# Performance work log

Hardware: AMD Instinct MI355X
Metric: run time of the kernel (lower is better)

## Reference

```python
import jax, jax.numpy as jnp
import numpy as np

N_HEADS, N_LEVELS, N_POINTS, D_MODEL = 8, 3, 12, 64
PARAM_NAMES = ['vp0_w','vp0_b','vp1_w','vp1_b','so0_w','so0_b','so1_w','so1_b','so2_w','so2_b','so3_w','so3_b','aw0_w','aw0_b','aw1_w','aw1_b','aw2_w','aw2_b','aw3_w','aw3_b','op0_w','op0_b','op1_w','op1_b']

def _lrelu(x):
    return jnp.where(x >= 0, x, 0.1 * x)

def _conv(x, w, b):
    y = jax.lax.conv_general_dilated(x, w, (1, 1), 'SAME', dimension_numbers=('NCHW', 'OIHW', 'NCHW'))
    return y + b[None, :, None, None]

def _bilinear(img, px, py):
    # img [B,C,H,W]; px,py [B,Q] absolute pixel coords; zero padding (grid_sample 'zeros')
    B, C, H, W = img.shape
    flat = img.reshape(B, C, H * W)
    x0 = jnp.floor(px); y0 = jnp.floor(py)
    wx1 = px - x0; wy1 = py - y0
    def g(xi, yi, wgt):
        valid = (xi >= 0) & (xi <= W - 1) & (yi >= 0) & (yi <= H - 1)
        xi_c = jnp.clip(xi, 0, W - 1).astype(jnp.int32)
        yi_c = jnp.clip(yi, 0, H - 1).astype(jnp.int32)
        v = jnp.take_along_axis(flat, (yi_c * W + xi_c)[:, None, :], axis=2)
        return v * (wgt * valid)[:, None, :]
    return (g(x0, y0, (1 - wx1) * (1 - wy1)) + g(x0 + 1, y0, wx1 * (1 - wy1))
          + g(x0, y0 + 1, (1 - wx1) * wy1) + g(x0 + 1, y0 + 1, wx1 * wy1))

def _flow_warp(img, flow):
    # img [n,C,h,w]; flow [n,2,h,w] (x,y); matches grid_sample align_corners=True
    n, C, h, w = img.shape
    gy, gx = jnp.meshgrid(jnp.arange(h, dtype=img.dtype), jnp.arange(w, dtype=img.dtype), indexing='ij')
    px = (gx[None] + flow[:, 0]).reshape(n, h * w)
    py = (gy[None] + flow[:, 1]).reshape(n, h * w)
    return _bilinear(img, px, py).reshape(n, C, h, w)

def _forward(x, flow_1, flow_2, flip_flow_1, flip_flow_2, p):
    n, t, c, h, w = x.shape
    hw = h * w; THW = t * hw
    M, L, P, D = N_HEADS, N_LEVELS, N_POINTS, c // N_HEADS
    flow_cn1 = flow_1
    flow_cn2 = flow_1 + _flow_warp(flow_2, flow_1)
    flow_n1c, flow_n1n2 = flip_flow_1, flow_2
    flow_n2n1 = flip_flow_2
    flow_n2c = flip_flow_2 + _flow_warp(flip_flow_1, flip_flow_2)
    warp_cn1 = _flow_warp(x[:, 1], flow_cn1)
    warp_cn2 = _flow_warp(x[:, 2], flow_cn2)
    warp_n1c = _flow_warp(x[:, 0], flow_n1c)
    warp_n1n2 = _flow_warp(x[:, 2], flow_n1n2)
    warp_n2n1 = _flow_warp(x[:, 1], flow_n2n1)
    warp_n2c = _flow_warp(x[:, 0], flow_n2c)
    extra = jnp.concatenate([x[:, 0], warp_cn1, warp_cn2, warp_n1c, warp_n1n2, warp_n2n1, warp_n2c,
                             flow_cn1, flow_cn2, flow_n1c, flow_n1n2, flow_n2n1, flow_n2c], axis=1)
    value = _conv(_lrelu(_conv(x.reshape(n, t * c, h, w), p['vp0_w'], p['vp0_b'])), p['vp1_w'], p['vp1_b'])
    def head(e, pre):
        y = _lrelu(_conv(e, p[pre + '0_w'], p[pre + '0_b']))
        y = _lrelu(_conv(y, p[pre + '1_w'], p[pre + '1_b']))
        y = _lrelu(_conv(y, p[pre + '2_w'], p[pre + '2_b']))
        return _conv(y, p[pre + '3_w'], p[pre + '3_b'])
    so = head(extra, 'so')  # [n, L*M*L*P*2, h, w]
    aw = head(extra, 'aw')  # [n, L*M*L*P*9, h, w]
    so = so.reshape(n, t, -1, hw).transpose(0, 1, 3, 2).reshape(n, THW, M, L, P, 2)
    aw = aw.reshape(n, t, -1, hw).transpose(0, 1, 3, 2).reshape(n, THW, M, L * P * 9)
    aw = jax.nn.softmax(aw, axis=-1).reshape(n, THW, M, L, P * 9)
    # flow-guided offsets: add per-(query-frame, target-level) flow to learned offsets
    off = so.reshape(n, t, hw, M, L, P, 2)
    fz = jnp.zeros_like(flow_cn2)
    def lvl(f0, f1, f2):
        s = jnp.stack([f0, f1, f2], 1)  # [n,3,2,h,w]
        return s.transpose(0, 3, 4, 1, 2).reshape(n, hw, L, 2)[:, None, :, None, :, None, :]
    off = jnp.concatenate([
        off[:, 0:1] + lvl(fz, flow_cn1, flow_cn2),
        off[:, 1:2] + lvl(flow_n1c, fz, flow_n1n2),
        off[:, 2:3] + lvl(flow_n2c, flow_n2n1, fz)], axis=1).reshape(n, THW, M, L, P, 2)
    # 3x3 integer patch around each sampling point
    pi, pj = jnp.meshgrid(jnp.arange(-1, 2), jnp.arange(-1, 2), indexing='ij')
    patch = jnp.stack([pi, pj], -1).reshape(1, 1, 1, 1, 1, 9, 2).astype(off.dtype)
    off = (off[..., None, :] + patch).reshape(n, THW, M, L, P * 9, 2)
    # reference points (valid_ratios are all 1: full masks are zeros)
    ry, rx = jnp.meshgrid((jnp.arange(h) + 0.5) / h, (jnp.arange(w) + 0.5) / w, indexing='ij')
    ref = jnp.stack([rx, ry], -1).reshape(1, hw, 2).astype(off.dtype)
    ref = jnp.tile(ref, (1, t, 1))  # [1, THW, 2]
    norm = jnp.array([w, h], dtype=off.dtype)
    loc = ref[:, :, None, None, None, :] + off / norm  # [n,THW,M,L,P*9,2] normalized
    # multi-scale deformable attention (all L levels share (h,w)); align_corners=False, zeros pad
    P9 = P * 9
    v = value.reshape(n, t, c, hw).transpose(0, 1, 3, 2).reshape(n, THW, M, D)
    vl = v.reshape(n, L, hw, M, D).transpose(0, 3, 1, 4, 2).reshape(n * M * L, D, h, w)
    px = (loc[..., 0] * w - 0.5).transpose(0, 2, 3, 1, 4).reshape(n * M * L, THW * P9)
    py = (loc[..., 1] * h - 0.5).transpose(0, 2, 3, 1, 4).reshape(n * M * L, THW * P9)
    sampled = _bilinear(vl, px, py).reshape(n, M, L, D, THW, P9)
    out = jnp.einsum('nmldqp,nqmlp->nqmd', sampled, aw).reshape(n, THW, c)
    out = out.reshape(n, t, h, w, c).transpose(0, 1, 4, 2, 3).reshape(n, t * c, h, w)
    out = _conv(_lrelu(_conv(out, p['op0_w'], p['op0_b'])), p['op1_w'], p['op1_b'])
    return out.reshape(n, t, c, h, w) + x

def setup_inputs():
    key = jax.random.key(0)
    n, t, c, h, w = 1, 3, 64, 32, 32
    ks = jax.random.split(key, 24)
    d = {}
    d['x'] = jax.random.normal(ks[0], (n, t, c, h, w), jnp.float32)
    for i, name in enumerate(['flow_1', 'flow_2', 'flip_flow_1', 'flip_flow_2']):
        d[name] = jax.random.normal(ks[1 + i], (n, 2, h, w), jnp.float32)
    cin_extra = 7 * c + 12
    specs = [('vp0', t * c, t * c), ('vp1', t * c, t * c),
             ('so0', c, cin_extra), ('so1', c, c), ('so2', c, c), ('so3', N_LEVELS * N_HEADS * N_LEVELS * N_POINTS * 2, c),
             ('aw0', c, cin_extra), ('aw1', c, c), ('aw2', c, c), ('aw3', N_LEVELS * N_HEADS * N_LEVELS * N_POINTS * 9, c),
             ('op0', t * c, t * c), ('op1', t * c, t * c)]
    for i, (name, co, ci) in enumerate(specs):
        kw, kb = jax.random.split(ks[5 + i])
        std = (2.0 / (ci * 9)) ** 0.5
        d[name + '_w'] = jax.random.normal(kw, (co, ci, 3, 3), jnp.float32) * std
        d[name + '_b'] = jax.random.normal(kb, (co,), jnp.float32) * 0.01
    return d

def reference(x, flow_1, flow_2, flip_flow_1, flip_flow_2, vp0_w, vp0_b, vp1_w, vp1_b, so0_w, so0_b, so1_w, so1_b, so2_w, so2_b, so3_w, so3_b, aw0_w, aw0_b, aw1_w, aw1_b, aw2_w, aw2_b, aw3_w, aw3_b, op0_w, op0_b, op1_w, op1_b):
    p = dict(zip(PARAM_NAMES, (vp0_w, vp0_b, vp1_w, vp1_b, so0_w, so0_b, so1_w, so1_b, so2_w, so2_b, so3_w, so3_b, aw0_w, aw0_b, aw1_w, aw1_b, aw2_w, aw2_b, aw3_w, aw3_b, op0_w, op0_b, op1_w, op1_b)))
    return _forward(x, flow_1, flow_2, flip_flow_1, flip_flow_2, p)
```

## Files before the change

### kernel.cpp

```cpp
#include <hip/hip_runtime.h>
#include <math.h>

#define HW 1024

typedef __attribute__((ext_vector_type(8))) short bf16x8;
typedef __attribute__((ext_vector_type(4))) float floatx4;

__device__ __forceinline__ unsigned short f2bf(float f) {
    unsigned u = __float_as_uint(f);
    u += 0x7FFF + ((u >> 16) & 1);
    return (unsigned short)(u >> 16);
}
__device__ __forceinline__ float bf2f(unsigned short u) {
    return __uint_as_float(((unsigned)u) << 16);
}
__device__ __forceinline__ float bflo(unsigned u) { return __uint_as_float(u << 16); }
__device__ __forceinline__ float bfhi(unsigned u) { return __uint_as_float(u & 0xffff0000u); }

__device__ __forceinline__ float bilin32(const float* __restrict__ img, float px, float py) {
    float x0f = floorf(px), y0f = floorf(py);
    float wx = px - x0f, wy = py - y0f;
    bool vx0 = (x0f >= 0.f) && (x0f <= 31.f);
    bool vx1 = (x0f >= -1.f) && (x0f <= 30.f);
    bool vy0 = (y0f >= 0.f) && (y0f <= 31.f);
    bool vy1 = (y0f >= -1.f) && (y0f <= 30.f);
    int ix0 = (int)fminf(fmaxf(x0f, 0.f), 31.f);
    int iy0 = (int)fminf(fmaxf(y0f, 0.f), 31.f);
    int ix1 = (int)fminf(fmaxf(x0f + 1.f, 0.f), 31.f);
    int iy1 = (int)fminf(fmaxf(y0f + 1.f, 0.f), 31.f);
    float w00 = (1.f - wx) * (1.f - wy) * ((vx0 && vy0) ? 1.f : 0.f);
    float w01 = wx * (1.f - wy) * ((vx1 && vy0) ? 1.f : 0.f);
    float w10 = (1.f - wx) * wy * ((vx0 && vy1) ? 1.f : 0.f);
    float w11 = wx * wy * ((vx1 && vy1) ? 1.f : 0.f);
    return w00 * img[iy0 * 32 + ix0] + w01 * img[iy0 * 32 + ix1] +
           w10 * img[iy1 * 32 + ix0] + w11 * img[iy1 * 32 + ix1];
}

__device__ __forceinline__ float2 comp_flow(const float* __restrict__ fa,
                                            const float* __restrict__ fb, int pix) {
    int y = pix >> 5, x = pix & 31;
    float fx = fa[pix], fy = fa[HW + pix];
    float px = (float)x + fx, py = (float)y + fy;
    float2 r;
    r.x = fx + bilin32(fb, px, py);
    r.y = fy + bilin32(fb + HW, px, py);
    return r;
}

struct WD { const float* src; int cout, Cin, nCb, wbase, beg; };
struct PrepP {
    const float *x, *f1, *f2, *ff1, *ff2;
    float *fcn2, *fn2c;
    unsigned short *x_pad, *extra_pad, *wgt;
    WD wd[12];
};

__global__ __launch_bounds__(256) void prep_k(PrepP P) {
    __shared__ float wlds[16 * 288];
    const int b = blockIdx.x, tid = threadIdx.x;
    if (b < 192) {
        int idx = b * 256 + tid;
        int pix = idx / 48, c4 = idx - pix * 48;
        int y = pix >> 5, xx = pix & 31;
        int c0 = c4 * 4;
        ushort4 s;
        s.x = f2bf(P.x[(size_t)(c0 + 0) * HW + pix]);
        s.y = f2bf(P.x[(size_t)(c0 + 1) * HW + pix]);
        s.z = f2bf(P.x[(size_t)(c0 + 2) * HW + pix]);
        s.w = f2bf(P.x[(size_t)(c0 + 3) * HW + pix]);
        *(ushort4*)(&P.x_pad[(size_t)((y + 1) * 34 + xx + 1) * 192 + c0]) = s;
    } else if (b < 2112) {
        int idx = (b - 192) * 256 + tid;
        int ch = idx >> 10, pix = idx & 1023;
        int y = pix >> 5, xx = pix & 31;
        float v = 0.f;
        if (ch < 64) {
            v = P.x[(size_t)ch * HW + pix];
        } else if (ch < 448) {
            int grp = (ch - 64) >> 6;
            int c = (ch - 64) & 63;
            const float* src;
            float fx, fy;
            if (grp == 0)      { src = P.x + 64 * HW;  fx = P.f1[pix];  fy = P.f1[HW + pix]; }
            else if (grp == 1) { src = P.x + 128 * HW; float2 r = comp_flow(P.f1, P.f2, pix);  fx = r.x; fy = r.y; }
            else if (grp == 2) { src = P.x;            fx = P.ff1[pix]; fy = P.ff1[HW + pix]; }
            else if (grp == 3) { src = P.x + 128 * HW; fx = P.f2[pix];  fy = P.f2[HW + pix]; }
            else if (grp == 4) { src = P.x + 64 * HW;  fx = P.ff2[pix]; fy = P.ff2[HW + pix]; }
            else               { src = P.x;            float2 r = comp_flow(P.ff2, P.ff1, pix); fx = r.x; fy = r.y; }
            v = bilin32(src + c * HW, (float)xx + fx, (float)y + fy);
        } else if (ch < 460) {
            int fc = ch - 448;
            int which = fc >> 1, comp = fc & 1;
            if (which == 0)      v = P.f1[comp * HW + pix];
            else if (which == 1) { float2 r = comp_flow(P.f1, P.f2, pix);  v = comp ? r.y : r.x; }
            else if (which == 2) v = P.ff1[comp * HW + pix];
            else if (which == 3) v = P.f2[comp * HW + pix];
            else if (which == 4) v = P.ff2[comp * HW + pix];
            else                 { float2 r = comp_flow(P.ff2, P.ff1, pix); v = comp ? r.y : r.x; }
        }
        P.extra_pad[(size_t)((y + 1) * 34 + xx + 1) * 480 + ch] = f2bf(v);
    } else if (b < 2128) {
        int idx = (b - 2112) * 256 + tid;
        if (idx < 1024) {
            float2 r = comp_flow(P.f1, P.f2, idx);
            P.fcn2[idx] = r.x; P.fcn2[HW + idx] = r.y;
        } else if (idx < 2048) {
            int pix = idx - 1024;
            float2 r = comp_flow(P.ff2, P.ff1, pix);
            P.fn2c[pix] = r.x; P.fn2c[HW + pix] = r.y;
        }
    } else if (b < 2144) {
        const int chans[9] = {192, 192, 480, 64, 64, 64, 64, 192, 192};
        size_t offs[9]; size_t a = 0;
        for (int i = 0; i < 9; ++i) { offs[i] = a; a += (size_t)1156 * chans[i]; }
        int bb = b - 2128;
        for (int item = bb; item < 9 * 132; item += 16) {
            int buf = item / 132, i = item - buf * 132;
            int py, px;
            if (i < 34) { py = 0; px = i; }
            else if (i < 68) { py = 33; px = i - 34; }
            else { int j = i - 68; py = 1 + (j >> 1); px = (j & 1) ? 33 : 0; }
            int C = chans[buf];
            unsigned short* p = P.x_pad + offs[buf] + (size_t)(py * 34 + px) * C;
            for (int c = tid; c < C; c += 256) p[c] = 0;
        }
    } else {
        int blk = b - 2144;
        int di = 0;
        while (di < 11 && blk >= P.wd[di + 1].beg) ++di;
        WD w = P.wd[di];
        int local = blk - w.beg;
        int co16 = local / w.nCb, cb = local - co16 * w.nCb;
        int cr0 = co16 * 16, ci0 = cb * 32;
        for (int i = tid; i < 16 * 288; i += 256) {
            int cr = i / 288, o = i - cr * 288;
            int crg = cr0 + cr, ci = ci0 + o / 9;
            float v = (crg < w.cout && ci < w.Cin)
                ? w.src[((size_t)crg * w.Cin + ci0) * 9 + o] : 0.f;
            wlds[i] = v;
        }
        __syncthreads();
        for (int e = tid; e < 9 * 512; e += 256) {
            int t = e >> 9, idx = e & 511;
            int j = idx & 7, lane = idx >> 3, q = lane >> 4, mm = lane & 15;
            P.wgt[((size_t)w.wbase + ((size_t)co16 * 9 + t) * w.nCb + cb) * 512 + idx] =
                f2bf(wlds[mm * 288 + (q * 8 + j) * 9 + t]);
        }
    }
}

struct CDesc {
    const unsigned short* in;
    const unsigned short* wgt;
    const float* bias;
    void* out;
    const float* residual;
    int Cpad, nCb, Cout, mode, cmod, relu, Mblocks;
};
struct CParam { CDesc d[4]; };

template<int PIXROWS, int COBLK>
__global__ __launch_bounds__(256) void conv_mfma_k(CParam P) {
    constexpr int TROWS = PIXROWS + 2;
    constexpr int TC = TROWS * 34 * 4;
    constexpr int ITRIPS = (TC + 255) / 256;
    constexpr int NTY = PIXROWS / 4;
    constexpr int NACC = NTY * 2;
    constexpr int MT = COBLK / 16;
    constexpr int WN = MT * 9 * 64;
    constexpr int WTRIPS = (WN + 255) / 256;
    __shared__ unsigned short blds[TROWS * 34 * 40];
    __shared__ unsigned short wlds[MT * 9 * 512];

    int bx = blockIdx.x;
    int di = 0;
    while (bx >= P.d[di].Mblocks) { bx -= P.d[di].Mblocks; ++di; }
    const CDesc d = P.d[di];

    const int tid = threadIdx.x;
    const int w = tid >> 6, lane = tid & 63;
    const int lq = lane >> 4, ln = lane & 15;
    const int co0 = bx * COBLK;
    const int by = blockIdx.y, y0 = by * PIXROWS;
    const unsigned short* __restrict__ in = d.in;
    const unsigned short* __restrict__ wg = d.wgt;
    const int Cpad = d.Cpad, nCb = d.nCb;

    floatx4 acc[MT][NACC];
#pragma unroll
    for (int mt = 0; mt < MT; ++mt)
#pragma unroll
        for (int nt = 0; nt < NACC; ++nt)
            acc[mt][nt] = (floatx4){0.f, 0.f, 0.f, 0.f};

    bf16x8 ireg[ITRIPS];
    bf16x8 wreg[WTRIPS];

    auto load_regs = [&](int cb) {
        const int ci0 = cb << 5;
#pragma unroll
        for (int k = 0; k < ITRIPS; ++k) {
            int i = tid + k * 256;
            if (i < TC) {
                int r = i / 136, rem = i - r * 136, c = rem >> 2, g = rem & 3;
                ireg[k] = *(const bf16x8*)(in + (size_t)((y0 + r) * 34 + c) * Cpad + ci0 + g * 8);
            }
        }
#pragma unroll
        for (int k = 0; k < WTRIPS; ++k) {
            int i = tid + k * 256;
            if (i < WN) {
                int chunk = i >> 6, l16 = i & 63;
                int mt = chunk / 9, t = chunk - mt * 9;
                wreg[k] = *(const bf16x8*)(wg + ((size_t)(((co0 >> 4) + mt) * 9 + t) * nCb + cb) * 512 + l16 * 8);
            }
        }
// ... 55 lines not shown
            const int pix = by * (PIXROWS * 32) + (w * NTY + ty) * 32 + tx * 16 + ln;
            float v[4];
#pragma unroll
            for (int r = 0; r < 4; ++r) {
                float vv = acc[mt][nt][r] + bv[r];
                if (d.relu) vv = (vv >= 0.f) ? vv : 0.1f * vv;
                v[r] = vv;
            }
            if (d.mode == 0) {
                float* o = (float*)d.out;
#pragma unroll
                for (int r = 0; r < 4; ++r) {
                    float vv = v[r];
                    if (d.residual) vv += d.residual[(size_t)(co + r) * HW + pix];
                    o[(size_t)(co + r) * HW + pix] = vv;
                }
            } else if (d.mode == 1) {
                int fq = co / d.cmod, cc = co - fq * d.cmod;
                *(float4*)((float*)d.out + ((size_t)fq * HW + pix) * d.cmod + cc) =
                    make_float4(v[0], v[1], v[2], v[3]);
            } else if (d.mode == 2) {
                int fq = co / d.cmod, cc = co - fq * d.cmod;
                ushort4 s4;
                s4.x = f2bf(v[0]); s4.y = f2bf(v[1]); s4.z = f2bf(v[2]); s4.w = f2bf(v[3]);
                *(ushort4*)((unsigned short*)d.out + ((size_t)fq * HW + pix) * d.cmod + cc) = s4;
            } else {
                int yy = (pix >> 5) + 1, xx = (pix & 31) + 1;
                ushort4 s4;
                s4.x = f2bf(v[0]); s4.y = f2bf(v[1]); s4.z = f2bf(v[2]); s4.w = f2bf(v[3]);
                *(ushort4*)((unsigned short*)d.out + (size_t)(yy * 34 + xx) * d.cmod + co) = s4;
            }
        }
    }
}

__global__ __launch_bounds__(256) void deform_attn_k(
    const unsigned short* __restrict__ value_b, const float* __restrict__ so_t,
    const unsigned short* __restrict__ aw_t,
    const float* __restrict__ flow_1, const float* __restrict__ flow_2,
    const float* __restrict__ flip_flow_1, const float* __restrict__ flip_flow_2,
    const float* __restrict__ flow_cn2, const float* __restrict__ flow_n2c,
    unsigned short* __restrict__ attn_pad)
{
    __shared__ unsigned short vlds[24576];
    __shared__ unsigned short pwlds[4][432];
    const int tid = threadIdx.x;
    const int wav = tid >> 6, lane = tid & 63;
    const int m = blockIdx.x & 7, qc = blockIdx.x >> 3;

    for (int i = tid; i < 3072; i += 256) {
        int l = i >> 10, p = i & 1023;
        *(bf16x8*)(&vlds[(size_t)i * 8]) =
            *(const bf16x8*)(value_b + ((size_t)((l * 8 + m) * 1024) + p) * 8);
    }
    __syncthreads();

    const int pp = lane & 15, gq = lane >> 4;
    const int gdy = (gq >> 1) * 2 - 1;
    const int gdx = (gq & 1) * 2 - 1;
    const bool selx = (gq & 1);
    const bool sely = (gq >> 1);

    for (int r = 0; r < 8; ++r) {
        const int q = qc * 32 + r * 4 + wav;
        const int f = q >> 10, pix = q & 1023;
        const int y = pix >> 5, x = pix & 31;

        float flx0 = 0.f, fly0 = 0.f, flx1 = 0.f, fly1 = 0.f, flx2 = 0.f, fly2 = 0.f;
        if (f == 0) {
            flx1 = flow_1[pix];      fly1 = flow_1[HW + pix];
            flx2 = flow_cn2[pix];    fly2 = flow_cn2[HW + pix];
        } else if (f == 1) {
            flx0 = flip_flow_1[pix]; fly0 = flip_flow_1[HW + pix];
            flx2 = flow_2[pix];      fly2 = flow_2[HW + pix];
        } else {
            flx0 = flow_n2c[pix];    fly0 = flow_n2c[HW + pix];
            flx1 = flip_flow_2[pix]; fly1 = flip_flow_2[HW + pix];
        }

        const unsigned short* awp = aw_t + (size_t)q * 2592 + m * 324;
        float av[6];
        float vmax = -1e30f;
// ... 86 lines not shown
                        int px = min(max(x0 + dx, 0), 31);
                        int py = min(max(y0 + dy, 0), 31);
                        float c = cg[sy][sx] * (v ? 1.f : 0.f);
                        uint4 vv = *(const uint4*)(&vlds[(size_t)(vbase + py * 32 + px) * 8]);
                        acc[0] = fmaf(c, bflo(vv.x), acc[0]);
                        acc[1] = fmaf(c, bfhi(vv.x), acc[1]);
                        acc[2] = fmaf(c, bflo(vv.y), acc[2]);
                        acc[3] = fmaf(c, bfhi(vv.y), acc[3]);
                        acc[4] = fmaf(c, bflo(vv.z), acc[4]);
                        acc[5] = fmaf(c, bfhi(vv.z), acc[5]);
                        acc[6] = fmaf(c, bflo(vv.w), acc[6]);
                        acc[7] = fmaf(c, bfhi(vv.w), acc[7]);
                    }
                }
            }
        }

#pragma unroll
        for (int dd = 0; dd < 8; ++dd) {
#pragma unroll
            for (int off = 32; off; off >>= 1) acc[dd] += __shfl_xor(acc[dd], off);
        }
        if (lane == 0) {
            unsigned short* op = attn_pad + (size_t)((y + 1) * 34 + x + 1) * 192 + f * 64 + m * 8;
            ushort4 s0, s1;
            s0.x = f2bf(acc[0]); s0.y = f2bf(acc[1]); s0.z = f2bf(acc[2]); s0.w = f2bf(acc[3]);
            s1.x = f2bf(acc[4]); s1.y = f2bf(acc[5]); s1.z = f2bf(acc[6]); s1.w = f2bf(acc[7]);
            *(ushort4*)(op) = s0;
            *(ushort4*)(op + 4) = s1;
        }
    }
}

extern "C" void kernel_launch(void* const* d_in, const int* in_sizes, int n_in,
                              void* d_out, int out_size, void* d_ws, size_t ws_size,
                              hipStream_t stream) {
    const float* x      = (const float*)d_in[0];
    const float* flow_1 = (const float*)d_in[1];
    const float* flow_2 = (const float*)d_in[2];
    const float* flip_1 = (const float*)d_in[3];
    const float* flip_2 = (const float*)d_in[4];
    const float* vp0_w = (const float*)d_in[5];  const float* vp0_b = (const float*)d_in[6];
    const float* vp1_w = (const float*)d_in[7];  const float* vp1_b = (const float*)d_in[8];
    const float* so0_w = (const float*)d_in[9];  const float* so0_b = (const float*)d_in[10];
    const float* so1_w = (const float*)d_in[11]; const float* so1_b = (const float*)d_in[12];
    const float* so2_w = (const float*)d_in[13]; const float* so2_b = (const float*)d_in[14];
    const float* so3_w = (const float*)d_in[15]; const float* so3_b = (const float*)d_in[16];
    const float* aw0_w = (const float*)d_in[17]; const float* aw0_b = (const float*)d_in[18];
    const float* aw1_w = (const float*)d_in[19]; const float* aw1_b = (const float*)d_in[20];
    const float* aw2_w = (const float*)d_in[21]; const float* aw2_b = (const float*)d_in[22];
    const float* aw3_w = (const float*)d_in[23]; const float* aw3_b = (const float*)d_in[24];
    const float* op0_w = (const float*)d_in[25]; const float* op0_b = (const float*)d_in[26];
    const float* op1_w = (const float*)d_in[27]; const float* op1_b = (const float*)d_in[28];
    float* out = (float*)d_out;
    (void)ws_size; (void)in_sizes; (void)n_in; (void)out_size;

    float* fws = (float*)d_ws;
    float* flow_cn2 = fws;
    float* flow_n2c = flow_cn2 + 2048;
    unsigned short* value_b = (unsigned short*)(flow_n2c + 2048);
    float* so_t     = (float*)(value_b + 196608);
    unsigned short* uws = (unsigned short*)(so_t + 1769472);
    unsigned short* x_pad     = uws;
    unsigned short* vp0h      = x_pad + 1156 * 192;
    unsigned short* extra_pad = vp0h + 1156 * 192;
    unsigned short* s1 = extra_pad + 1156 * 480;
    unsigned short* a1 = s1 + 1156 * 64;
    unsigned short* s2 = a1 + 1156 * 64;
    unsigned short* a2 = s2 + 1156 * 64;
    unsigned short* attn_pad = a2 + 1156 * 64;
    unsigned short* op0h     = attn_pad + 1156 * 192;
    unsigned short* aw_t = op0h + 1156 * 192;
    unsigned short* wgt  = aw_t + (size_t)3072 * 2592;

    PrepP pp;
    pp.x = x; pp.f1 = flow_1; pp.f2 = flow_2; pp.ff1 = flip_1; pp.ff2 = flip_2;
    pp.fcn2 = flow_cn2; pp.fn2c = flow_n2c;
    pp.x_pad = x_pad; pp.extra_pad = extra_pad; pp.wgt = wgt;
    pp.wd[0]  = {vp0_w, 192, 192, 6,     0,    0};
    pp.wd[1]  = {vp1_w, 192, 192, 6,   648,   72};
    pp.wd[2]  = {so0_w,  64, 460, 15, 1296,  144};
    pp.wd[3]  = {aw0_w,  64, 460, 15, 1836,  204};
    pp.wd[4]  = {so1_w,  64,  64, 2,  2376,  264};
    pp.wd[5]  = {aw1_w,  64,  64, 2,  2448,  272};
    pp.wd[6]  = {so2_w,  64,  64, 2,  2520,  280};
    pp.wd[7]  = {aw2_w,  64,  64, 2,  2592,  288};
    pp.wd[8]  = {so3_w, 1728, 64, 2,  2664,  296};
    pp.wd[9]  = {aw3_w, 7776, 64, 2,  4608,  512};
    pp.wd[10] = {op0_w, 192, 192, 6, 13392, 1488};
    pp.wd[11] = {op1_w, 192, 192, 6, 14040, 1560};
    prep_k<<<3776, 256, 0, stream>>>(pp);

    const int BIG = 1 << 30;
    CDesc nul = {nullptr, nullptr, nullptr, nullptr, nullptr, 0, 0, 0, 0, 0, 0, BIG};

    {
        CParam cp;
        cp.d[0] = {x_pad,     wgt + (size_t)0 * 512,    vp0_b, vp0h, nullptr, 192, 6,  192, 3, 192, 1, 12};
        cp.d[1] = {extra_pad, wgt + (size_t)1296 * 512, so0_b, s1,   nullptr, 480, 15, 64,  3, 64,  1, 4};
        cp.d[2] = {extra_pad, wgt + (size_t)1836 * 512, aw0_b, a1,   nullptr, 480, 15, 64,  3, 64,  1, 4};
        cp.d[3] = nul;
        conv_mfma_k<4, 16><<<dim3(20, 8), 256, 0, stream>>>(cp);
    }
    {
        CParam cp;
        cp.d[0] = {vp0h, wgt + (size_t)648 * 512,  vp1_b, value_b, nullptr, 192, 6, 192, 2, 8,  0, 12};
        cp.d[1] = {s1,   wgt + (size_t)2376 * 512, so1_b, s2,      nullptr, 64,  2, 64,  3, 64, 1, 4};
        cp.d[2] = {a1,   wgt + (size_t)2448 * 512, aw1_b, a2,      nullptr, 64,  2, 64,  3, 64, 1, 4};
        cp.d[3] = nul;
        conv_mfma_k<4, 16><<<dim3(20, 8), 256, 0, stream>>>(cp);
    }
    {
        CParam cp;
        cp.d[0] = {s2, wgt + (size_t)2520 * 512, so2_b, s1, nullptr, 64, 2, 64, 3, 64, 1, 4};
        cp.d[1] = {a2, wgt + (size_t)2592 * 512, aw2_b, a1, nullptr, 64, 2, 64, 3, 64, 1, 4};
        cp.d[2] = nul; cp.d[3] = nul;
        conv_mfma_k<4, 16><<<dim3(8, 8), 256, 0, stream>>>(cp);
    }
    {
        CParam cp;
        cp.d[0] = {s1, wgt + (size_t)2664 * 512, so3_b, so_t, nullptr, 64, 2, 1728, 1, 576,  0, 27};
        cp.d[1] = {a1, wgt + (size_t)4608 * 512, aw3_b, aw_t, nullptr, 64, 2, 7776, 2, 2592, 0, 122};
        cp.d[2] = nul; cp.d[3] = nul;
        conv_mfma_k<8, 64><<<dim3(149, 4), 256, 0, stream>>>(cp);
    }

    deform_attn_k<<<768, 256, 0, stream>>>(value_b, so_t, aw_t,
                                           flow_1, flow_2, flip_1, flip_2,
                                           flow_cn2, flow_n2c, attn_pad);

    {
        CParam cp;
        cp.d[0] = {attn_pad, wgt + (size_t)13392 * 512, op0_b, op0h, nullptr, 192, 6, 192, 3, 192, 1, 12};
        cp.d[1] = nul; cp.d[2] = nul; cp.d[3] = nul;
        conv_mfma_k<4, 16><<<dim3(12, 8), 256, 0, stream>>>(cp);
    }
    {
        CParam cp;
        cp.d[0] = {op0h, wgt + (size_t)14040 * 512, op1_b, out, x, 192, 6, 192, 0, 0, 0, 12};
        cp.d[1] = nul; cp.d[2] = nul; cp.d[3] = nul;
        conv_mfma_k<4, 16><<<dim3(12, 8), 256, 0, stream>>>(cp);
    }
}
```

Before: 269.9 us.

## Fuse all stages into persistent megakernel with software grid barriers

```diff
diff --git a/kernel.cpp b/kernel.cpp
--- a/kernel.cpp
+++ b/kernel.cpp
@@ -2,6 +2,8 @@
 #include <math.h>
 
 #define HW 1024
+#define GRID 768
+#define SMEM_BYTES 52608
 
 typedef __attribute__((ext_vector_type(8))) short bf16x8;
 typedef __attribute__((ext_vector_type(4))) float floatx4;
@@ -47,67 +49,82 @@
     return r;
 }
 
-struct WD { const float* src; int cout, Cin, nCb, wbase, beg; };
-struct PrepP {
-    const float *x, *f1, *f2, *ff1, *ff2;
-    float *fcn2, *fn2c;
-    unsigned short *x_pad, *extra_pad, *wgt;
-    WD wd[12];
+struct MegaA {
+    const float* x;
+    const float* f1; const float* f2; const float* ff1; const float* ff2;
+    const float* wp[24];
+    float* out;
+    char* ws;
+    int* bar;
 };
 
-__global__ __launch_bounds__(256) void prep_k(PrepP P) {
-    __shared__ float wlds[16 * 288];
-    const int b = blockIdx.x, tid = threadIdx.x;
+__device__ __forceinline__ void grid_bar(int* bar, int phase) {
+    __syncthreads();
+    if (threadIdx.x == 0) {
+        __threadfence();
+        __hip_atomic_fetch_add(bar + phase * 16, 1, __ATOMIC_ACQ_REL, __HIP_MEMORY_SCOPE_AGENT);
+        while (__hip_atomic_load(bar + phase * 16, __ATOMIC_RELAXED, __HIP_MEMORY_SCOPE_AGENT) < GRID)
+            __builtin_amdgcn_s_sleep(8);
+        __threadfence();
+    }
+    __syncthreads();
+}
+
+__device__ __forceinline__ void prep_tile(const MegaA& A, float* fcn2, float* fn2c,
+                                          unsigned short* x_pad, unsigned short* extra_pad,
+                                          unsigned short* wgt, int b, char* smraw) {
+    const int tid = threadIdx.x;
+    const float* x = A.x;
     if (b < 192) {
         int idx = b * 256 + tid;
         int pix = idx / 48, c4 = idx - pix * 48;
         int y = pix >> 5, xx = pix & 31;
         int c0 = c4 * 4;
         ushort4 s;
-        s.x = f2bf(P.x[(size_t)(c0 + 0) * HW + pix]);
-        s.y = f2bf(P.x[(size_t)(c0 + 1) * HW + pix]);
-        s.z = f2bf(P.x[(size_t)(c0 + 2) * HW + pix]);
-        s.w = f2bf(P.x[(size_t)(c0 + 3) * HW + pix]);
-        *(ushort4*)(&P.x_pad[(size_t)((y + 1) * 34 + xx + 1) * 192 + c0]) = s;
+        s.x = f2bf(x[(size_t)(c0 + 0) * HW + pix]);
+        s.y = f2bf(x[(size_t)(c0 + 1) * HW + pix]);
+        s.z = f2bf(x[(size_t)(c0 + 2) * HW + pix]);
+        s.w = f2bf(x[(size_t)(c0 + 3) * HW + pix]);
+        *(ushort4*)(&x_pad[(size_t)((y + 1) * 34 + xx + 1) * 192 + c0]) = s;
     } else if (b < 2112) {
         int idx = (b - 192) * 256 + tid;
         int ch = idx >> 10, pix = idx & 1023;
         int y = pix >> 5, xx = pix & 31;
         float v = 0.f;
         if (ch < 64) {
-            v = P.x[(size_t)ch * HW + pix];
+            v = x[(size_t)ch * HW + pix];
         } else if (ch < 448) {
             int grp = (ch - 64) >> 6;
             int c = (ch - 64) & 63;
             const float* src;
             float fx, fy;
-            if (grp == 0)      { src = P.x + 64 * HW;  fx = P.f1[pix];  fy = P.f1[HW + pix]; }
-            else if (grp == 1) { src = P.x + 128 * HW; float2 r = comp_flow(P.f1, P.f2, pix);  fx = r.x; fy = r.y; }
-            else if (grp == 2) { src = P.x;            fx = P.ff1[pix]; fy = P.ff1[HW + pix]; }
-            else if (grp == 3) { src = P.x + 128 * HW; fx = P.f2[pix];  fy = P.f2[HW + pix]; }
-            else if (grp == 4) { src = P.x + 64 * HW;  fx = P.ff2[pix]; fy = P.ff2[HW + pix]; }
-            else               { src = P.x;            float2 r = comp_flow(P.ff2, P.ff1, pix); fx = r.x; fy = r.y; }
+            if (grp == 0)      { src = x + 64 * HW;  fx = A.f1[pix];  fy = A.f1[HW + pix]; }
+            else if (grp == 1) { src = x + 128 * HW; float2 r = comp_flow(A.f1, A.f2, pix);  fx = r.x; fy = r.y; }
+            else if (grp == 2) { src = x;            fx = A.ff1[pix]; fy = A.ff1[HW + pix]; }
+            else if (grp == 3) { src = x + 128 * HW; fx = A.f2[pix];  fy = A.f2[HW + pix]; }
+            else if (grp == 4) { src = x + 64 * HW;  fx = A.ff2[pix]; fy = A.ff2[HW + pix]; }
+            else               { src = x;            float2 r = comp_flow(A.ff2, A.ff1, pix); fx = r.x; fy = r.y; }
             v = bilin32(src + c * HW, (float)xx + fx, (float)y + fy);
         } else if (ch < 460) {
             int fc = ch - 448;
             int which = fc >> 1, comp = fc & 1;
-            if (which == 0)      v = P.f1[comp * HW + pix];
-            else if (which == 1) { float2 r = comp_flow(P.f1, P.f2, pix);  v = comp ? r.y : r.x; }
-            else if (which == 2) v = P.ff1[comp * HW + pix];
-            else if (which == 3) v = P.f2[comp * HW + pix];
-            else if (which == 4) v = P.ff2[comp * HW + pix];
-            else                 { float2 r = comp_flow(P.ff2, P.ff1, pix); v = comp ? r.y : r.x; }
-        }
-        P.extra_pad[(size_t)((y + 1) * 34 + xx + 1) * 480 + ch] = f2bf(v);
+            if (which == 0)      v = A.f1[comp * HW + pix];
+            else if (which == 1) { float2 r = comp_flow(A.f1, A.f2, pix);  v = comp ? r.y : r.x; }
+            else if (which == 2) v = A.ff1[comp * HW + pix];
+            else if (which == 3) v = A.f2[comp * HW + pix];
+            else if (which == 4) v = A.ff2[comp * HW + pix];
+            else                 { float2 r = comp_flow(A.ff2, A.ff1, pix); v = comp ? r.y : r.x; }
+        }
+        extra_pad[(size_t)((y + 1) * 34 + xx + 1) * 480 + ch] = f2bf(v);
     } else if (b < 2128) {
         int idx = (b - 2112) * 256 + tid;
         if (idx < 1024) {
-            float2 r = comp_flow(P.f1, P.f2, idx);
-            P.fcn2[idx] = r.x; P.fcn2[HW + idx] = r.y;
+            float2 r = comp_flow(A.f1, A.f2, idx);
+            fcn2[idx] = r.x; fcn2[HW + idx] = r.y;
         } else if (idx < 2048) {
             int pix = idx - 1024;
-            float2 r = comp_flow(P.ff2, P.ff1, pix);
-            P.fn2c[pix] = r.x; P.fn2c[HW + pix] = r.y;
+            float2 r = comp_flow(A.ff2, A.ff1, pix);
+            fn2c[pix] = r.x; fn2c[HW + pix] = r.y;
         }
     } else if (b < 2144) {
         const int chans[9] = {192, 192, 480, 64, 64, 64, 64, 192, 192};
@@ -121,29 +138,45 @@
             else if (i < 68) { py = 33; px = i - 34; }
             else { int j = i - 68; py = 1 + (j >> 1); px = (j & 1) ? 33 : 0; }
             int C = chans[buf];
-            unsigned short* p = P.x_pad + offs[buf] + (size_t)(py * 34 + px) * C;
+            unsigned short* p = x_pad + offs[buf] + (size_t)(py * 34 + px) * C;
             for (int c = tid; c < C; c += 256) p[c] = 0;
         }
     } else {
+        float* wlds = (float*)smraw;
         int blk = b - 2144;
+        const int wcout[12] = {192,192,64,64,64,64,64,64,1728,7776,192,192};
+        const int wcin[12]  = {192,192,460,460,64,64,64,64,64,64,192,192};
+        const int wnCb[12]  = {6,6,15,15,2,2,2,2,2,2,6,6};
+        const int wbase[12] = {0,648,1296,1836,2376,2448,2520,2592,2664,4608,13392,14040};
+        const int wbeg[12]  = {0,72,144,204,264,272,280,288,296,512,1488,1560};
         int di = 0;
-        while (di < 11 && blk >= P.wd[di + 1].beg) ++di;
-        WD w = P.wd[di];
-        int local = blk - w.beg;
-        int co16 = local / w.nCb, cb = local - co16 * w.nCb;
+        while (di < 11 && blk >= wbeg[di + 1]) ++di;
+        const float* wsrc;
+        switch (di) {
+            case 0: wsrc = A.wp[0]; break;  case 1: wsrc = A.wp[2]; break;
+            case 2: wsrc = A.wp[4]; break;  case 3: wsrc = A.wp[12]; break;
+            case 4: wsrc = A.wp[6]; break;  case 5: wsrc = A.wp[14]; break;
+            case 6: wsrc = A.wp[8]; break;  case 7: wsrc = A.wp[16]; break;
+            case 8: wsrc = A.wp[10]; break; case 9: wsrc = A.wp[18]; break;
+            case 10: wsrc = A.wp[20]; break; default: wsrc = A.wp[22]; break;
+        }
+        int cout = wcout[di], Cin = wcin[di], nCb = wnCb[di];
+        int local = blk - wbeg[di];
+        int co16 = local / nCb, cb = local - co16 * nCb;
         int cr0 = co16 * 16, ci0 = cb * 32;
+        __syncthreads();
         for (int i = tid; i < 16 * 288; i += 256) {
             int cr = i / 288, o = i - cr * 288;
             int crg = cr0 + cr, ci = ci0 + o / 9;
-            float v = (crg < w.cout && ci < w.Cin)
-                ? w.src[((size_t)crg * w.Cin + ci0) * 9 + o] : 0.f;
+            float v = (crg < cout && ci < Cin)
+                ? wsrc[((size_t)crg * Cin + ci0) * 9 + o] : 0.f;
             wlds[i] = v;
         }
         __syncthreads();
         for (int e = tid; e < 9 * 512; e += 256) {
             int t = e >> 9, idx = e & 511;
             int j = idx & 7, lane = idx >> 3, q = lane >> 4, mm = lane & 15;
-            P.wgt[((size_t)w.wbase + ((size_t)co16 * 9 + t) * w.nCb + cb) * 512 + idx] =
+            wgt[((size_t)wbase[di] + ((size_t)co16 * 9 + t) * nCb + cb) * 512 + idx] =
                 f2bf(wlds[mm * 288 + (q * 8 + j) * 9 + t]);
         }
     }
@@ -155,12 +188,11 @@
     const float* bias;
     void* out;
     const float* residual;
-    int Cpad, nCb, Cout, mode, cmod, relu, Mblocks;
+    int Cpad, nCb, Cout, mode, cmod, relu;
 };
-struct CParam { CDesc d[4]; };
 
 template<int PIXROWS, int COBLK>
-__global__ __launch_bounds__(256) void conv_mfma_k(CParam P) {
+__device__ __forceinline__ void conv_tile(const CDesc d, int bx, int by, char* smraw) {
     constexpr int TROWS = PIXROWS + 2;
     constexpr int TC = TROWS * 34 * 4;
     constexpr int ITRIPS = (TC + 255) / 256;
@@ -169,19 +201,14 @@
     constexpr int MT = COBLK / 16;
     constexpr int WN = MT * 9 * 64;
     constexpr int WTRIPS = (WN + 255) / 256;
-    __shared__ unsigned short blds[TROWS * 34 * 40];
-    __shared__ unsigned short wlds[MT * 9 * 512];
-
-    int bx = blockIdx.x;
-    int di = 0;
-    while (bx >= P.d[di].Mblocks) { bx -= P.d[di].Mblocks; ++di; }
-    const CDesc d = P.d[di];
+    unsigned short* blds = (unsigned short*)smraw;
+    unsigned short* wlds = (unsigned short*)(smraw + TROWS * 34 * 40 * 2);
 
     const int tid = threadIdx.x;
     const int w = tid >> 6, lane = tid & 63;
     const int lq = lane >> 4, ln = lane & 15;
     const int co0 = bx * COBLK;
-    const int by = blockIdx.y, y0 = by * PIXROWS;
+    const int y0 = by * PIXROWS;
     const unsigned short* __restrict__ in = d.in;
     const unsigned short* __restrict__ wg = d.wgt;
     const int Cpad = d.Cpad, nCb = d.nCb;
@@ -305,20 +332,21 @@
     }
 }
 
-__global__ __launch_bounds__(256) void deform_attn_k(
+__device__ __forceinline__ void attn_tile(
     const unsigned short* __restrict__ value_b, const float* __restrict__ so_t,
     const unsigned short* __restrict__ aw_t,
     const float* __restrict__ flow_1, const float* __restrict__ flow_2,
     const float* __restrict__ flip_flow_1, const float* __restrict__ flip_flow_2,
     const float* __restrict__ flow_cn2, const float* __restrict__ flow_n2c,
-    unsigned short* __restrict__ attn_pad)
+    unsigned short* __restrict__ attn_pad, int vb, char* smraw)
 {
-    __shared__ unsigned short vlds[24576];
-    __shared__ unsigned short pwlds[4][432];
+    unsigned short* vlds = (unsigned short*)smraw;
+    unsigned short (*pwlds)[432] = (unsigned short(*)[432])(smraw + 49152);
     const int tid = threadIdx.x;
     const int wav = tid >> 6, lane = tid & 63;
-    const int m = blockIdx.x & 7, qc = blockIdx.x >> 3;
-
+    const int m = vb & 7, qc = vb >> 3;
+
+    __syncthreads();
     for (int i = tid; i < 3072; i += 256) {
         int l = i >> 10, p = i & 1023;
         *(bf16x8*)(&vlds[(size_t)i * 8]) =
@@ -471,36 +499,13 @@
     }
 }
 
-extern "C" void kernel_launch(void* const* d_in, const int* in_sizes, int n_in,
-                              void* d_out, int out_size, void* d_ws, size_t ws_size,
-                              hipStream_t stream) {
-    const float* x      = (const float*)d_in[0];
-    const float* flow_1 = (const float*)d_in[1];
-    const float* flow_2 = (const float*)d_in[2];
-    const float* flip_1 = (const float*)d_in[3];
-    const float* flip_2 = (const float*)d_in[4];
-    const float* vp0_w = (const float*)d_in[5];  const float* vp0_b = (const float*)d_in[6];
-    const float* vp1_w = (const float*)d_in[7];  const float* vp1_b = (const float*)d_in[8];
-    const float* so0_w = (const float*)d_in[9];  const float* so0_b = (const float*)d_in[10];
-    const float* so1_w = (const float*)d_in[11]; const float* so1_b = (const float*)d_in[12];
-    const float* so2_w = (const float*)d_in[13]; const float* so2_b = (const float*)d_in[14];
-    const float* so3_w = (const float*)d_in[15]; const float* so3_b = (const float*)d_in[16];
-    const float* aw0_w = (const float*)d_in[17]; const float* aw0_b = (const float*)d_in[18];
-    const float* aw1_w = (const float*)d_in[19]; const float* aw1_b = (const float*)d_in[20];
-    const float* aw2_w = (const float*)d_in[21]; const float* aw2_b = (const float*)d_in[22];
-    const float* aw3_w = (const float*)d_in[23]; const float* aw3_b = (const float*)d_in[24];
-    const float* op0_w = (const float*)d_in[25]; const float* op0_b = (const float*)d_in[26];
-    const float* op1_w = (const float*)d_in[27]; const float* op1_b = (const float*)d_in[28];
-    float* out = (float*)d_out;
-    (void)ws_size; (void)in_sizes; (void)n_in; (void)out_size;
-
-    float* fws = (float*)d_ws;
-    float* flow_cn2 = fws;
+__global__ __launch_bounds__(256, 3) void mega_k(MegaA A) {
+    __shared__ __align__(16) char sm[SMEM_BYTES];
+    float* flow_cn2 = (float*)A.ws;
     float* flow_n2c = flow_cn2 + 2048;
     unsigned short* value_b = (unsigned short*)(flow_n2c + 2048);
-    float* so_t     = (float*)(value_b + 196608);
-    unsigned short* uws = (unsigned short*)(so_t + 1769472);
-    unsigned short* x_pad     = uws;
+    float* so_t = (float*)(value_b + 196608);
+    unsigned short* x_pad = (unsigned short*)(so_t + 1769472);
     unsigned short* vp0h      = x_pad + 1156 * 192;
     unsigned short* extra_pad = vp0h + 1156 * 192;
     unsigned short* s1 = extra_pad + 1156 * 480;
@@ -508,76 +513,98 @@
     unsigned short* s2 = a1 + 1156 * 64;
     unsigned short* a2 = s2 + 1156 * 64;
     unsigned short* attn_pad = a2 + 1156 * 64;
-    unsigned short* op0h     = attn_pad + 1156 * 192;
+    unsigned short* op0h = attn_pad + 1156 * 192;
     unsigned short* aw_t = op0h + 1156 * 192;
-    unsigned short* wgt  = aw_t + (size_t)3072 * 2592;
-
-    PrepP pp;
-    pp.x = x; pp.f1 = flow_1; pp.f2 = flow_2; pp.ff1 = flip_1; pp.ff2 = flip_2;
-    pp.fcn2 = flow_cn2; pp.fn2c = flow_n2c;
-    pp.x_pad = x_pad; pp.extra_pad = extra_pad; pp.wgt = wgt;
-    pp.wd[0]  = {vp0_w, 192, 192, 6,     0,    0};
-    pp.wd[1]  = {vp1_w, 192, 192, 6,   648,   72};
-    pp.wd[2]  = {so0_w,  64, 460, 15, 1296,  144};
-    pp.wd[3]  = {aw0_w,  64, 460, 15, 1836,  204};
-    pp.wd[4]  = {so1_w,  64,  64, 2,  2376,  264};
-    pp.wd[5]  = {aw1_w,  64,  64, 2,  2448,  272};
-    pp.wd[6]  = {so2_w,  64,  64, 2,  2520,  280};
-    pp.wd[7]  = {aw2_w,  64,  64, 2,  2592,  288};
-    pp.wd[8]  = {so3_w, 1728, 64, 2,  2664,  296};
-    pp.wd[9]  = {aw3_w, 7776, 64, 2,  4608,  512};
-    pp.wd[10] = {op0_w, 192, 192, 6, 13392, 1488};
-    pp.wd[11] = {op1_w, 192, 192, 6, 14040, 1560};
-    prep_k<<<3776, 256, 0, stream>>>(pp);
-
-    const int BIG = 1 << 30;
-    CDesc nul = {nullptr, nullptr, nullptr, nullptr, nullptr, 0, 0, 0, 0, 0, 0, BIG};
-
-    {
-        CParam cp;
-        cp.d[0] = {x_pad,     wgt + (size_t)0 * 512,    vp0_b, vp0h, nullptr, 192, 6,  192, 3, 192, 1, 12};
-        cp.d[1] = {extra_pad, wgt + (size_t)1296 * 512, so0_b, s1,   nullptr, 480, 15, 64,  3, 64,  1, 4};
-        cp.d[2] = {extra_pad, wgt + (size_t)1836 * 512, aw0_b, a1,   nullptr, 480, 15, 64,  3, 64,  1, 4};
-        cp.d[3] = nul;
-        conv_mfma_k<4, 16><<<dim3(20, 8), 256, 0, stream>>>(cp);
-    }
-    {
-        CParam cp;
-        cp.d[0] = {vp0h, wgt + (size_t)648 * 512,  vp1_b, value_b, nullptr, 192, 6, 192, 2, 8,  0, 12};
-        cp.d[1] = {s1,   wgt + (size_t)2376 * 512, so1_b, s2,      nullptr, 64,  2, 64,  3, 64, 1, 4};
-        cp.d[2] = {a1,   wgt + (size_t)2448 * 512, aw1_b, a2,      nullptr, 64,  2, 64,  3, 64, 1, 4};
-        cp.d[3] = nul;
-        conv_mfma_k<4, 16><<<dim3(20, 8), 256, 0, stream>>>(cp);
-    }
-    {
-        CParam cp;
-        cp.d[0] = {s2, wgt + (size_t)2520 * 512, so2_b, s1, nullptr, 64, 2, 64, 3, 64, 1, 4};
-        cp.d[1] = {a2, wgt + (size_t)2592 * 512, aw2_b, a1, nullptr, 64, 2, 64, 3, 64, 1, 4};
-        cp.d[2] = nul; cp.d[3] = nul;
-        conv_mfma_k<4, 16><<<dim3(8, 8), 256, 0, stream>>>(cp);
-    }
-    {
-        CParam cp;
-        cp.d[0] = {s1, wgt + (size_t)2664 * 512, so3_b, so_t, nullptr, 64, 2, 1728, 1, 576,  0, 27};
-        cp.d[1] = {a1, wgt + (size_t)4608 * 512, aw3_b, aw_t, nullptr, 64, 2, 7776, 2, 2592, 0, 122};
-        cp.d[2] = nul; cp.d[3] = nul;
-        conv_mfma_k<8, 64><<<dim3(149, 4), 256, 0, stream>>>(cp);
-    }
-
-    deform_attn_k<<<768, 256, 0, stream>>>(value_b, so_t, aw_t,
-                                           flow_1, flow_2, flip_1, flip_2,
-                                           flow_cn2, flow_n2c, attn_pad);
-
-    {
-        CParam cp;
-        cp.d[0] = {attn_pad, wgt + (size_t)13392 * 512, op0_b, op0h, nullptr, 192, 6, 192, 3, 192, 1, 12};
-        cp.d[1] = nul; cp.d[2] = nul; cp.d[3] = nul;
-        conv_mfma_k<4, 16><<<dim3(12, 8), 256, 0, stream>>>(cp);
-    }
-    {
-        CParam cp;
-        cp.d[0] = {op0h, wgt + (size_t)14040 * 512, op1_b, out, x, 192, 6, 192, 0, 0, 0, 12};
-        cp.d[1] = nul; cp.d[2] = nul; cp.d[3] = nul;
-        conv_mfma_k<4, 16><<<dim3(12, 8), 256, 0, stream>>>(cp);
-    }
-}
+    unsigned short* wgt = aw_t + (size_t)3072 * 2592;
+    int* bar = A.bar;
+
+    for (int vb = blockIdx.x; vb < 3776; vb += GRID)
+        prep_tile(A, flow_cn2, flow_n2c, x_pad, extra_pad, wgt, vb, sm);
+    grid_bar(bar, 0);
+
+    for (int vb = blockIdx.x; vb < 160; vb += GRID) {
+        int bx = vb >> 3, by = vb & 7;
+        CDesc d;
+        if (bx < 12)      { d = {x_pad, wgt, A.wp[1], vp0h, nullptr, 192, 6, 192, 3, 192, 1}; }
+        else if (bx < 16) { d = {extra_pad, wgt + (size_t)1296 * 512, A.wp[13], a1, nullptr, 480, 15, 64, 3, 64, 1};
+                            d = {extra_pad, wgt + (size_t)1296 * 512, A.wp[5], s1, nullptr, 480, 15, 64, 3, 64, 1}; bx -= 12; }
+        else              { d = {extra_pad, wgt + (size_t)1836 * 512, A.wp[13], a1, nullptr, 480, 15, 64, 3, 64, 1}; bx -= 16; }
+        conv_tile<4, 16>(d, bx, by, sm);
+    }
+    grid_bar(bar, 1);
+
+    for (int vb = blockIdx.x; vb < 160; vb += GRID) {
+        int bx = vb >> 3, by = vb & 7;
+        CDesc d;
+        if (bx < 12)      { d = {vp0h, wgt + (size_t)648 * 512, A.wp[3], value_b, nullptr, 192, 6, 192, 2, 8, 0}; }
+        else if (bx < 16) { d = {s1, wgt + (size_t)2376 * 512, A.wp[7], s2, nullptr, 64, 2, 64, 3, 64, 1}; bx -= 12; }
+        else              { d = {a1, wgt + (size_t)2448 * 512, A.wp[15], a2, nullptr, 64, 2, 64, 3, 64, 1}; bx -= 16; }
+        conv_tile<4, 16>(d, bx, by, sm);
+    }
+    grid_bar(bar, 2);
+
+    for (int vb = blockIdx.x; vb < 64; vb += GRID) {
+        int bx = vb >> 3, by = vb & 7;
+        CDesc d;
+        if (bx < 4) { d = {s2, wgt + (size_t)2520 * 512, A.wp[9], s1, nullptr, 64, 2, 64, 3, 64, 1}; }
+        else        { d = {a2, wgt + (size_t)2592 * 512, A.wp[17], a1, nullptr, 64, 2, 64, 3, 64, 1}; bx -= 4; }
+        conv_tile<4, 16>(d, bx, by, sm);
+    }
+    grid_bar(bar, 3);
+
+    for (int vb = blockIdx.x; vb < 1188; vb += GRID) {
+        int bx = vb >> 2, by = vb & 3;
+        CDesc d;
+        if (bx < 54) { d = {s1, wgt + (size_t)2664 * 512, A.wp[11], so_t, nullptr, 64, 2, 1728, 1, 576, 0}; }
+        else         { d = {a1, wgt + (size_t)4608 * 512, A.wp[19], aw_t, nullptr, 64, 2, 7776, 2, 2592, 0}; bx -= 54; }
+        conv_tile<8, 32>(d, bx, by, sm);
+    }
+    grid_bar(bar, 4);
+
+    for (int vb = blockIdx.x; vb < 768; vb += GRID)
+        attn_tile(value_b, so_t, aw_t, A.f1, A.f2, A.ff1, A.ff2,
+                  flow_cn2, flow_n2c, attn_pad, vb, sm);
+    grid_bar(bar, 5);
+
+    for (int vb = blockIdx.x; vb < 96; vb += GRID) {
+        int bx = vb >> 3, by = vb & 7;
+        CDesc d = {attn_pad, wgt + (size_t)13392 * 512, A.wp[21], op0h, nullptr, 192, 6, 192, 3, 192, 1};
+        conv_tile<4, 16>(d, bx, by, sm);
+    }
+    grid_bar(bar, 6);
+
+    for (int vb = blockIdx.x; vb < 96; vb += GRID) {
+        int bx = vb >> 3, by = vb & 7;
+        CDesc d = {op0h, wgt + (size_t)14040 * 512, A.wp[23], A.out, A.x, 192, 6, 192, 0, 0, 0};
+        conv_tile<4, 16>(d, bx, by, sm);
+    }
+}
+
+extern "C" void kernel_launch(void* const* d_in, const int* in_sizes, int n_in,
+                              void* d_out, int out_size, void* d_ws, size_t ws_size,
+                              hipStream_t stream) {
+    (void)in_sizes; (void)n_in; (void)out_size; (void)ws_size;
+
+    MegaA A;
+    A.x   = (const float*)d_in[0];
+    A.f1  = (const float*)d_in[1];
+    A.f2  = (const float*)d_in[2];
+    A.ff1 = (const float*)d_in[3];
+    A.ff2 = (const float*)d_in[4];
+    for (int i = 0; i < 24; ++i) A.wp[i] = (const float*)d_in[5 + i];
+    A.out = (float*)d_out;
+    A.ws  = (char*)d_ws;
+
+    size_t off = 0;
+    off += (size_t)4096 * 4;
+    off += (size_t)196608 * 2;
+    off += (size_t)1769472 * 4;
+    off += (size_t)1156 * 1504 * 2;
+    off += (size_t)3072 * 2592 * 2;
+    off += (size_t)14688 * 512 * 2;
+    int* bar = (int*)(A.ws + off);
+    A.bar = bar;
+
+    hipMemsetAsync(bar, 0, 8 * 16 * sizeof(int), stream);
+    hipLaunchKernelGGL(mega_k, dim3(GRID), dim3(256), 0, stream, A);
+}
```

After: 800.0 us. +196.4%, slower.

## Fuse so1/so2 and aw1/aw2 conv pairs into one kernel with vp1

Applied to the files above, without the earlier changes.

```diff
diff --git a/kernel.cpp b/kernel.cpp
--- a/kernel.cpp
+++ b/kernel.cpp
@@ -160,7 +160,7 @@
 struct CParam { CDesc d[4]; };
 
 template<int PIXROWS, int COBLK>
-__global__ __launch_bounds__(256) void conv_mfma_k(CParam P) {
+__device__ __forceinline__ void conv_tile(const CDesc d, int bx, int by, char* smraw) {
     constexpr int TROWS = PIXROWS + 2;
     constexpr int TC = TROWS * 34 * 4;
     constexpr int ITRIPS = (TC + 255) / 256;
@@ -169,19 +169,14 @@
     constexpr int MT = COBLK / 16;
     constexpr int WN = MT * 9 * 64;
     constexpr int WTRIPS = (WN + 255) / 256;
-    __shared__ unsigned short blds[TROWS * 34 * 40];
-    __shared__ unsigned short wlds[MT * 9 * 512];
-
-    int bx = blockIdx.x;
-    int di = 0;
-    while (bx >= P.d[di].Mblocks) { bx -= P.d[di].Mblocks; ++di; }
-    const CDesc d = P.d[di];
+    unsigned short* blds = (unsigned short*)smraw;
+    unsigned short* wlds = (unsigned short*)(smraw + TROWS * 34 * 40 * 2);
 
     const int tid = threadIdx.x;
     const int w = tid >> 6, lane = tid & 63;
     const int lq = lane >> 4, ln = lane & 15;
     const int co0 = bx * COBLK;
-    const int by = blockIdx.y, y0 = by * PIXROWS;
+    const int y0 = by * PIXROWS;
     const unsigned short* __restrict__ in = d.in;
     const unsigned short* __restrict__ wg = d.wgt;
     const int Cpad = d.Cpad, nCb = d.nCb;
@@ -303,6 +298,171 @@
             }
         }
     }
+}
+
+template<int PIXROWS, int COBLK>
+__global__ __launch_bounds__(256) void conv_mfma_k(CParam P) {
+    constexpr int TROWS = PIXROWS + 2;
+    constexpr int MT = COBLK / 16;
+    __shared__ __align__(16) char sm[TROWS * 34 * 40 * 2 + MT * 9 * 512 * 2];
+    int bx = blockIdx.x;
+    int di = 0;
+    while (bx >= P.d[di].Mblocks) { bx -= P.d[di].Mblocks; ++di; }
+    conv_tile<PIXROWS, COBLK>(P.d[di], bx, blockIdx.y, sm);
+}
+
+struct FDesc {
+    const unsigned short* in;
+    const unsigned short* w1;
+    const float* b1;
+    const unsigned short* w2;
+    const float* b2;
+    unsigned short* out;
+};
+
+__device__ __forceinline__ void fused2_tile(const FDesc d, int by, char* smraw) {
+    unsigned short* blds = (unsigned short*)smraw;
+    unsigned short* ilds = (unsigned short*)(smraw + 21760);
+    unsigned short* wlds = (unsigned short*)(smraw + 21760 + 29376);
+    const int tid = threadIdx.x;
+    const int w = tid >> 6, lane = tid & 63;
+    const int lq = lane >> 4, ln = lane & 15;
+    const int y0 = by * 4;
+
+    floatx4 acc1[4][3];
+#pragma unroll
+    for (int mt = 0; mt < 4; ++mt)
+#pragma unroll
+        for (int nt = 0; nt < 3; ++nt)
+            acc1[mt][nt] = (floatx4){0.f, 0.f, 0.f, 0.f};
+
+    for (int cb = 0; cb < 2; ++cb) {
+        __syncthreads();
+        for (int i = tid; i < 1088; i += 256) {
+            int r = i / 136, rem = i - r * 136, c = rem >> 2, g = rem & 3;
+            int pr = min(max(y0 - 1 + r, 0), 33);
+            *(bf16x8*)(&blds[(r * 34 + c) * 40 + g * 8]) =
+                *(const bf16x8*)(d.in + (size_t)(pr * 34 + c) * 64 + cb * 32 + g * 8);
+        }
+        for (int i = tid; i < 2304; i += 256) {
+            int chunk = i >> 6, l16 = i & 63;
+            int mt = chunk / 9, t = chunk - mt * 9;
+            *(bf16x8*)(&wlds[chunk * 512 + l16 * 8]) =
+                *(const bf16x8*)(d.w1 + ((size_t)(mt * 9 + t) * 2 + cb) * 512 + l16 * 8);
+        }
+        __syncthreads();
+        for (int t = 0; t < 9; ++t) {
+            int dy = t / 3, dx = t - dy * 3;
+            bf16x8 bfr[3];
+#pragma unroll
+            for (int nt = 0; nt < 3; ++nt) {
+                int p = (w * 3 + nt) * 16 + ln;
+                int r = p >> 5, col = p & 31;
+                bfr[nt] = *(const bf16x8*)(&blds[((r + dy) * 34 + col + dx) * 40 + lq * 8]);
+            }
+#pragma unroll
+            for (int mt = 0; mt < 4; ++mt) {
+                bf16x8 afr = *(const bf16x8*)(&wlds[(mt * 9 + t) * 512 + lane * 8]);
+#pragma unroll
+                for (int nt = 0; nt < 3; ++nt)
+                    acc1[mt][nt] = __builtin_amdgcn_mfma_f32_16x16x32_bf16(afr, bfr[nt], acc1[mt][nt], 0, 0, 0);
+            }
+        }
+    }
+    __syncthreads();
+    for (int i = tid; i < 192; i += 256) {
+        int rr = i / 32, rem = i - rr * 32;
+        int side = rem >> 4, c4 = rem & 15;
+        int col = side ? 33 : 0;
+        ushort4 z; z.x = 0; z.y = 0; z.z = 0; z.w = 0;
+        *(ushort4*)(&ilds[(rr * 34 + col) * 72 + c4 * 4]) = z;
+    }
+#pragma unroll
+    for (int mt = 0; mt < 4; ++mt) {
+        int co = mt * 16 + lq * 4;
+        float bv[4];
+#pragma unroll
+        for (int r = 0; r < 4; ++r) bv[r] = d.b1[co + r];
+#pragma unroll
+        for (int nt = 0; nt < 3; ++nt) {
+            int p = (w * 3 + nt) * 16 + ln;
+            int r = p >> 5, col = p & 31;
+            int yi = y0 - 1 + r;
+            float msk = (yi >= 0 && yi <= 31) ? 1.f : 0.f;
+            ushort4 s4;
+            float v0 = acc1[mt][nt][0] + bv[0]; v0 = (v0 >= 0.f) ? v0 : 0.1f * v0;
+            float v1 = acc1[mt][nt][1] + bv[1]; v1 = (v1 >= 0.f) ? v1 : 0.1f * v1;
+            float v2 = acc1[mt][nt][2] + bv[2]; v2 = (v2 >= 0.f) ? v2 : 0.1f * v2;
+            float v3 = acc1[mt][nt][3] + bv[3]; v3 = (v3 >= 0.f) ? v3 : 0.1f * v3;
+            s4.x = f2bf(v0 * msk); s4.y = f2bf(v1 * msk);
+            s4.z = f2bf(v2 * msk); s4.w = f2bf(v3 * msk);
+            *(ushort4*)(&ilds[(r * 34 + col + 1) * 72 + co]) = s4;
+        }
+    }
+    __syncthreads();
+
+    floatx4 acc2[4][2];
+#pragma unroll
+    for (int mt = 0; mt < 4; ++mt)
+#pragma unroll
+        for (int nt = 0; nt < 2; ++nt)
+            acc2[mt][nt] = (floatx4){0.f, 0.f, 0.f, 0.f};
+
+    for (int cb = 0; cb < 2; ++cb) {
+        __syncthreads();
+        for (int i = tid; i < 2304; i += 256) {
+            int chunk = i >> 6, l16 = i & 63;
+            int mt = chunk / 9, t = chunk - mt * 9;
+            *(bf16x8*)(&wlds[chunk * 512 + l16 * 8]) =
+                *(const bf16x8*)(d.w2 + ((size_t)(mt * 9 + t) * 2 + cb) * 512 + l16 * 8);
+        }
+        __syncthreads();
+        for (int t = 0; t < 9; ++t) {
+            int dy = t / 3, dx = t - dy * 3;
+            bf16x8 bfr[2];
+#pragma unroll
+            for (int nt = 0; nt < 2; ++nt) {
+                int col = nt * 16 + ln;
+                int r = w + dy;
+                bfr[nt] = *(const bf16x8*)(&ilds[(r * 34 + col + dx) * 72 + cb * 32 + lq * 8]);
+            }
+#pragma unroll
+            for (int mt = 0; mt < 4; ++mt) {
+                bf16x8 afr = *(const bf16x8*)(&wlds[(mt * 9 + t) * 512 + lane * 8]);
+#pragma unroll
+                for (int nt = 0; nt < 2; ++nt)
+                    acc2[mt][nt] = __builtin_amdgcn_mfma_f32_16x16x32_bf16(afr, bfr[nt], acc2[mt][nt], 0, 0, 0);
+            }
+        }
+    }
+#pragma unroll
+    for (int mt = 0; mt < 4; ++mt) {
+        int co = mt * 16 + lq * 4;
+        float bv[4];
+#pragma unroll
+        for (int r = 0; r < 4; ++r) bv[r] = d.b2[co + r];
+#pragma unroll
+        for (int nt = 0; nt < 2; ++nt) {
+            int col = nt * 16 + ln;
+            int yo = y0 + w;
+            ushort4 s4;
+            float v0 = acc2[mt][nt][0] + bv[0]; v0 = (v0 >= 0.f) ? v0 : 0.1f * v0;
+            float v1 = acc2[mt][nt][1] + bv[1]; v1 = (v1 >= 0.f) ? v1 : 0.1f * v1;
+            float v2 = acc2[mt][nt][2] + bv[2]; v2 = (v2 >= 0.f) ? v2 : 0.1f * v2;
+            float v3 = acc2[mt][nt][3] + bv[3]; v3 = (v3 >= 0.f) ? v3 : 0.1f * v3;
+            s4.x = f2bf(v0); s4.y = f2bf(v1); s4.z = f2bf(v2); s4.w = f2bf(v3);
+            *(ushort4*)(&d.out[(size_t)((yo + 1) * 34 + col + 1) * 64 + co]) = s4;
+        }
+    }
+}
+
+struct L2FParam { CDesc vp1; FDesc so; FDesc aw; };
+
+__global__ __launch_bounds__(256) void l2f_k(L2FParam P) {
+    __shared__ __align__(16) char sm[21760 + 29376 + 36864];
+    if (blockIdx.x < 12)       conv_tile<4, 16>(P.vp1, blockIdx.x, blockIdx.y, sm);
+    else if (blockIdx.x == 12) fused2_tile(P.so, blockIdx.y, sm);
+    else                       fused2_tile(P.aw, blockIdx.y, sm);
 }
 
 __global__ __launch_bounds__(256) void deform_attn_k(
@@ -542,24 +702,16 @@
         conv_mfma_k<4, 16><<<dim3(20, 8), 256, 0, stream>>>(cp);
     }
     {
-        CParam cp;
-        cp.d[0] = {vp0h, wgt + (size_t)648 * 512,  vp1_b, value_b, nullptr, 192, 6, 192, 2, 8,  0, 12};
-        cp.d[1] = {s1,   wgt + (size_t)2376 * 512, so1_b, s2,      nullptr, 64,  2, 64,  3, 64, 1, 4};
-        cp.d[2] = {a1,   wgt + (size_t)2448 * 512, aw1_b, a2,      nullptr, 64,  2, 64,  3, 64, 1, 4};
-        cp.d[3] = nul;
-        conv_mfma_k<4, 16><<<dim3(20, 8), 256, 0, stream>>>(cp);
+        L2FParam lp;
+        lp.vp1 = {vp0h, wgt + (size_t)648 * 512, vp1_b, value_b, nullptr, 192, 6, 192, 2, 8, 0, 12};
+        lp.so  = {s1, wgt + (size_t)2376 * 512, so1_b, wgt + (size_t)2520 * 512, so2_b, s2};
+        lp.aw  = {a1, wgt + (size_t)2448 * 512, aw1_b, wgt + (size_t)2592 * 512, aw2_b, a2};
+        l2f_k<<<dim3(14, 8), 256, 0, stream>>>(lp);
     }
     {
         CParam cp;
-        cp.d[0] = {s2, wgt + (size_t)2520 * 512, so2_b, s1, nullptr, 64, 2, 64, 3, 64, 1, 4};
-        cp.d[1] = {a2, wgt + (size_t)2592 * 512, aw2_b, a1, nullptr, 64, 2, 64, 3, 64, 1, 4};
-        cp.d[2] = nul; cp.d[3] = nul;
-        conv_mfma_k<4, 16><<<dim3(8, 8), 256, 0, stream>>>(cp);
-    }
-    {
-        CParam cp;
-        cp.d[0] = {s1, wgt + (size_t)2664 * 512, so3_b, so_t, nullptr, 64, 2, 1728, 1, 576,  0, 27};
-        cp.d[1] = {a1, wgt + (size_t)4608 * 512, aw3_b, aw_t, nullptr, 64, 2, 7776, 2, 2592, 0, 122};
+        cp.d[0] = {s2, wgt + (size_t)2664 * 512, so3_b, so_t, nullptr, 64, 2, 1728, 1, 576,  0, 27};
+        cp.d[1] = {a2, wgt + (size_t)4608 * 512, aw3_b, aw_t, nullptr, 64, 2, 7776, 2, 2592, 0, 122};
         cp.d[2] = nul; cp.d[3] = nul;
         conv_mfma_k<8, 64><<<dim3(149, 4), 256, 0, stream>>>(cp);
     }
```

Result: slower. 284.2 us (+5.3%).
